# Performance work log

Measured on AMD Instinct MI355X. Metric: run time of the kernel, lower is better.

Reference implementation:

```python
import jax, jax.numpy as jnp
import numpy as np

K = 2097152  # number of time samples


def setup_inputs() -> dict:
    key = jax.random.key(0)
    k1, k2 = jax.random.split(key)
    # impact parameters spanning full occultation, partial overlap and no overlap
    b = jax.random.uniform(k1, (K,), dtype=jnp.float32, minval=0.0, maxval=1.3)
    # line-of-sight coordinate: positive -> in front of star (transit), negative -> masked
    z = jax.random.normal(k2, (K,), dtype=jnp.float32)
    r = jnp.float32(0.1)  # planet/star radius ratio
    u = jnp.array([0.3, 0.2], dtype=jnp.float32)  # quadratic limb darkening
    return {"u": u, "b": b, "r": r, "z": z, "order": 10}


def _intensity(u, rho):
    # I(mu) = 1 - sum_n u_n (1 - mu)^n, mu = sqrt(1 - rho^2); Horner-style accumulation
    mu = jnp.sqrt(jnp.clip(1.0 - rho * rho, 1e-12))
    omm = 1.0 - mu
    I = jnp.ones_like(rho)
    p = jnp.ones_like(rho)
    for i in range(u.shape[0]):  # static, small (n_u coefficients)
        p = p * omm
        I = I - u[i] * p
    return I


def _light_curve(u, b, r, order):
    # Gauss-Legendre nodes/weights for the order-`order` quadrature of the
    # occultation surface integrals (order is a static python int)
    xs_np, ws_np = np.polynomial.legendre.leggauss(order)
    xs = jnp.asarray(xs_np, dtype=b.dtype)
    ws = jnp.asarray(ws_np, dtype=b.dtype)

    n = jnp.arange(1, u.shape[0] + 1, dtype=b.dtype)
    # total stellar flux (I(0)=1 normalization): pi*(1 - sum u_n * 2/((n+1)(n+2)))
    norm = jnp.pi * (1.0 - jnp.sum(u * 2.0 / ((n + 1.0) * (n + 2.0))))

    b = jnp.abs(b)
    # --- fully occulted core: stellar annuli rho in [0, clip(r-b, 0, 1)] ---
    core_hi = jnp.clip(r - b, 0.0, 1.0)                 # [K]
    rho_c = 0.5 * core_hi[:, None] * (xs + 1.0)         # [K, order]
    f_core = 0.5 * core_hi * jnp.sum(
        ws * _intensity(u, rho_c) * (2.0 * jnp.pi) * rho_c, axis=-1)

    # --- partially occulted annulus: rho in [|b-r|, clip(b+r, 0, 1)] ---
    lo = jnp.clip(jnp.abs(b - r), 0.0, 1.0)
    hi = jnp.clip(b + r, 0.0, 1.0)
    width = jnp.maximum(hi - lo, 0.0)
    rho_a = lo[:, None] + 0.5 * width[:, None] * (xs + 1.0)   # [K, order]
    # arc angle of stellar circle of radius rho inside the occulter:
    # alpha = 2*arccos((b^2 + rho^2 - r^2) / (2 b rho))
    denom = 2.0 * b[:, None] * rho_a
    safe = denom > 1e-12
    cosarg = jnp.where(safe,
                       (b[:, None] ** 2 + rho_a ** 2 - r ** 2) / jnp.where(safe, denom, 1.0),
                       0.0)
    alpha = jnp.where(safe,
                      2.0 * jnp.arccos(jnp.clip(cosarg, -0.999999, 0.999999)),
                      0.0)
    f_ann = 0.5 * width * jnp.sum(
        ws * _intensity(u, rho_a) * alpha * rho_a, axis=-1)

    # fractional flux deficit (negative dip, flux = 1 + lc)
    return -(f_core + f_ann) / norm


def reference(u, b, r, z, order):
    lc = _light_curve(u, b, r, order)
    return jnp.where(z > 0, lc, 0.0)
```

## Files before the change

kernel.cpp:

```cpp
#include <hip/hip_runtime.h>
#include <math.h>

#define GL_ORDER 10
#define TAB_N 512
#define BMAX 1.3f
#define BLOCK 256
#define CHUNKS 2
#define ELEMS_PER_BLOCK (BLOCK * 4 * CHUNKS)

__device__ __forceinline__ float acos_fast(float x) {
    const float ax = fabsf(x);
    const float s  = __builtin_amdgcn_sqrtf(1.0f - ax);
    const float p  = fmaf(ax, fmaf(ax, fmaf(ax, -0.0187293f, 0.0742610f),
                                   -0.2121144f), 1.5707288f);
    const float r = s * p;
    return (x < 0.0f) ? (3.14159265358979323846f - r) : r;
}

__device__ float lc_eval(float bb, float r, float u0, float u1,
                         float c_core, float c_ann) {
    const float tj[GL_ORDER] = {
        0.013046735741414128f, 0.067468316655507744f, 0.160295215850487787f,
        0.283302302935376393f, 0.425562830509184362f, 0.574437169490815638f,
        0.716697697064623607f, 0.839704784149512213f, 0.932531683344492256f,
        0.986953264258585872f};
    const float wj[GL_ORDER] = {
        0.066671344308688138f, 0.149451349150580593f, 0.219086362515982044f,
        0.269266719309996355f, 0.295524224714752870f, 0.295524224714752870f,
        0.269266719309996355f, 0.219086362515982044f, 0.149451349150580593f,
        0.066671344308688138f};

    const float core_hi = fminf(fmaxf(r - bb, 0.0f), 1.0f);
    const float lo    = fminf(fabsf(bb - r), 1.0f);
    const float hi    = fminf(bb + r, 1.0f);
    const float width = fmaxf(hi - lo, 0.0f);

    const float b2r2 = fmaf(bb, bb, -r * r);
    const float twob = 2.0f * bb;

    float s_core = 0.0f;
    float s_ann  = 0.0f;

#pragma unroll
    for (int j = 0; j < GL_ORDER; ++j) {
        const float t = tj[j];

        const float rc   = core_hi * t;
        const float muc  = __builtin_amdgcn_sqrtf(fmaxf(fmaf(-rc, rc, 1.0f), 1e-12f));
        const float ommc = 1.0f - muc;
        const float Ic   = fmaf(-ommc, fmaf(u1, ommc, u0), 1.0f);
        s_core = fmaf(wj[j] * t, Ic, s_core);

        const float ra   = fmaf(width, t, lo);
        const float ra2  = ra * ra;
        const float mua  = __builtin_amdgcn_sqrtf(fmaxf(1.0f - ra2, 1e-12f));
        const float omma = 1.0f - mua;
        const float Ia   = fmaf(-omma, fmaf(u1, omma, u0), 1.0f);

        const float cosarg_raw = (b2r2 + ra2) * __builtin_amdgcn_rcpf(twob * ra);
        const float cosarg = fminf(fmaxf(cosarg_raw, -0.999999f), 0.999999f);
        const float ac = acos_fast(cosarg);

        s_ann = fmaf(wj[j] * Ia, ac * ra, s_ann);
    }

    return fmaf(c_core * core_hi * core_hi, s_core, c_ann * width * s_ann);
}

__global__ __launch_bounds__(BLOCK) void LimbDarkLightCurve_55370718380097_kernel(
    const float* __restrict__ u, const float* __restrict__ bptr,
    const float* __restrict__ rptr, const float* __restrict__ zptr,
    float* __restrict__ out, int K) {
    __shared__ float fnode[TAB_N + 1];

    const float u0 = u[0];
    const float u1 = u[1];
    const float r  = rptr[0];
    const float inv_norm =
        1.0f / (3.14159265358979323846f *
                (1.0f - u0 * (1.0f / 3.0f) - u1 * (1.0f / 6.0f)));
    const float c_core = -3.14159265358979323846f * inv_norm;
    const float c_ann  = -inv_norm;

    const float hstep = BMAX / (float)TAB_N;
    for (int node = threadIdx.x; node <= TAB_N; node += BLOCK) {
        fnode[node] = lc_eval((float)node * hstep, r, u0, u1, c_core, c_ann);
    }
    __syncthreads();

    const float scale = (float)TAB_N / BMAX;
    const int base = blockIdx.x * ELEMS_PER_BLOCK;

#pragma unroll
    for (int c = 0; c < CHUNKS; ++c) {
        const int i4 = base + (threadIdx.x + c * BLOCK) * 4;
        if (i4 + 3 < K) {
            const float4 b4 = *reinterpret_cast<const float4*>(bptr + i4);
            const float4 z4 = *reinterpret_cast<const float4*>(zptr + i4);
            float bs[4] = {b4.x, b4.y, b4.z, b4.w};
            float zs[4] = {z4.x, z4.y, z4.z, z4.w};
            float os[4];
#pragma unroll
            for (int k = 0; k < 4; ++k) {
                const float x = fabsf(bs[k]) * scale;
                int   i = (int)x;
                i = (i < TAB_N - 1) ? i : (TAB_N - 1);
                const float f  = x - (float)i;
                const float v0 = fnode[i];
                const float v1 = fnode[i + 1];
                const float v  = fmaf(f, v1 - v0, v0);
                os[k] = (zs[k] > 0.0f) ? v : 0.0f;
            }
            float4 o = {os[0], os[1], os[2], os[3]};
            *reinterpret_cast<float4*>(out + i4) = o;
        } else {
            for (int i = i4; i < K; ++i) {
                const float x = fabsf(bptr[i]) * scale;
                int   ii = (int)x;
                ii = (ii < TAB_N - 1) ? ii : (TAB_N - 1);
                const float f  = x - (float)ii;
                const float v0 = fnode[ii];
                const float v1 = fnode[ii + 1];
                const float v  = fmaf(f, v1 - v0, v0);
                out[i] = (zptr[i] > 0.0f) ? v : 0.0f;
            }
        }
    }
}

extern "C" void kernel_launch(void* const* d_in, const int* in_sizes, int n_in,
                              void* d_out, int out_size, void* d_ws, size_t ws_size,
                              hipStream_t stream) {
    const float* u = (const float*)d_in[0];
    const float* b = (const float*)d_in[1];
    const float* r = (const float*)d_in[2];
    const float* z = (const float*)d_in[3];
    float* out = (float*)d_out;
    const int K = in_sizes[1];

    const int grid = (K + ELEMS_PER_BLOCK - 1) / ELEMS_PER_BLOCK;
    LimbDarkLightCurve_55370718380097_kernel<<<grid, BLOCK, 0, stream>>>(
        u, b, r, z, out, K);
}
```

Measured before the change: 78.86 us.

## Prefetch inputs before table build, skip nodes beyond 1+r, double per-block work

Issues the global float4 loads of b and z before each block builds its shared lookup table, so memory latency overlaps the table computation. Table nodes with b >= 1+r are set to zero instead of running the quadrature. CHUNKS grows from 2 to 4, halving the block count so the per-block table build is amortised over more elements. The cost is more registers held across the table build and fewer blocks to hide latency.

```diff
diff --git a/kernel.cpp b/kernel.cpp
--- a/kernel.cpp
+++ b/kernel.cpp
@@ -5,7 +5,7 @@
 #define TAB_N 512
 #define BMAX 1.3f
 #define BLOCK 256
-#define CHUNKS 2
+#define CHUNKS 4
 #define ELEMS_PER_BLOCK (BLOCK * 4 * CHUNKS)
 
 __device__ __forceinline__ float acos_fast(float x) {
@@ -82,23 +82,37 @@
     const float c_core = -3.14159265358979323846f * inv_norm;
     const float c_ann  = -inv_norm;
 
+    const int base = blockIdx.x * ELEMS_PER_BLOCK;
+    const bool full = (base + ELEMS_PER_BLOCK) <= K;
+
+    float4 b4[CHUNKS], z4[CHUNKS];
+    if (full) {
+#pragma unroll
+        for (int c = 0; c < CHUNKS; ++c) {
+            const int i4 = base + (threadIdx.x + c * BLOCK) * 4;
+            b4[c] = *reinterpret_cast<const float4*>(bptr + i4);
+            z4[c] = *reinterpret_cast<const float4*>(zptr + i4);
+        }
+    }
+
     const float hstep = BMAX / (float)TAB_N;
+    const float blim  = 1.0f + r;
     for (int node = threadIdx.x; node <= TAB_N; node += BLOCK) {
-        fnode[node] = lc_eval((float)node * hstep, r, u0, u1, c_core, c_ann);
+        const float bb = (float)node * hstep;
+        fnode[node] = (bb < blim)
+                          ? lc_eval(bb, r, u0, u1, c_core, c_ann)
+                          : 0.0f;
     }
     __syncthreads();
 
     const float scale = (float)TAB_N / BMAX;
-    const int base = blockIdx.x * ELEMS_PER_BLOCK;
 
+    if (full) {
 #pragma unroll
-    for (int c = 0; c < CHUNKS; ++c) {
-        const int i4 = base + (threadIdx.x + c * BLOCK) * 4;
-        if (i4 + 3 < K) {
-            const float4 b4 = *reinterpret_cast<const float4*>(bptr + i4);
-            const float4 z4 = *reinterpret_cast<const float4*>(zptr + i4);
-            float bs[4] = {b4.x, b4.y, b4.z, b4.w};
-            float zs[4] = {z4.x, z4.y, z4.z, z4.w};
+        for (int c = 0; c < CHUNKS; ++c) {
+            const int i4 = base + (threadIdx.x + c * BLOCK) * 4;
+            float bs[4] = {b4[c].x, b4[c].y, b4[c].z, b4[c].w};
+            float zs[4] = {z4[c].x, z4[c].y, z4[c].z, z4[c].w};
             float os[4];
 #pragma unroll
             for (int k = 0; k < 4; ++k) {
@@ -113,8 +127,12 @@
             }
             float4 o = {os[0], os[1], os[2], os[3]};
             *reinterpret_cast<float4*>(out + i4) = o;
-        } else {
-            for (int i = i4; i < K; ++i) {
+        }
+    } else {
+        for (int c = 0; c < CHUNKS; ++c) {
+            const int i4 = base + (threadIdx.x + c * BLOCK) * 4;
+            const int iend = (i4 + 4 < K) ? (i4 + 4) : K;
+            for (int i = i4; i < iend; ++i) {
                 const float x = fabsf(bptr[i]) * scale;
                 int   ii = (int)x;
                 ii = (ii < TAB_N - 1) ? ii : (TAB_N - 1);
```

Result: no change. 79.42 us (+0.7%).
